# Kernel tuning notes

Hardware: AMD Instinct MI355X
Metric: run time of the kernel (lower is better)

## Reference

```python
import jax, jax.numpy as jnp
import numpy as np

B, T, D = 8, 4096, 1280   # batch, frames, feature dim
Q, K = 4, 256             # num_quantizers, codebook_size


def setup_inputs() -> dict:
    key = jax.random.key(0)
    k1, k2, k3 = jax.random.split(key, 3)
    z = jax.random.normal(k1, (B, T, D), jnp.float32)
    mask = jax.random.randint(k2, (B, T), 0, 2).astype(bool)
    codebooks = jax.random.normal(k3, (Q, K, D), jnp.float32)
    return {"z": z, "mask": mask, "codebooks": codebooks}


def _stage(residual, codebook):
    # squared L2 distance: ||r||^2 - 2 r.c + ||c||^2; ||r||^2 constant over codes -> drop for argmin
    dots = jnp.einsum('btd,kd->btk', residual, codebook)            # [B,T,K]
    d2 = jnp.sum(codebook * codebook, axis=-1) - 2.0 * dots          # [B,T,K]
    idx = jnp.argmin(d2, axis=-1)                                    # [B,T]
    q = codebook[idx]                                                # gather -> [B,T,D]
    return idx, q


def reference(z, mask, codebooks):
    residual = z
    quantized_out = jnp.zeros_like(z)
    commit = jnp.zeros((), z.dtype)
    mf = mask.astype(z.dtype)                                        # [B,T]
    denom = jnp.maximum(jnp.sum(mf), 1.0)
    indices = []
    for qi in range(codebooks.shape[0]):
        idx, q = _stage(residual, codebooks[qi])
        q_sg = jax.lax.stop_gradient(q)
        # straight-through estimator, as in vector-quantize-pytorch
        q_st = residual + jax.lax.stop_gradient(q - residual)
        quantized_out = quantized_out + q_st
        # masked commitment loss (MSE to detached codes, averaged over valid frames)
        se = jnp.mean((residual - q_sg) ** 2, axis=-1)               # [B,T]
        commit = commit + jnp.sum(se * mf) / denom
        # residual for next stage uses detached quantized (EMA codebooks)
        residual = residual - q_sg
        indices.append(idx)
    indices = jnp.stack(indices, axis=-1)                            # [B,T,Q]
    return quantized_out, indices, commit
```

## Files before the change

### kernel.cpp

```cpp
#include <hip/hip_runtime.h>
#include <hip/hip_bf16.h>
#include <float.h>

#define ROWS 32768
#define D4 320
#define QQ 4
#define KK 256
#define QUANT_N (ROWS*1280)
#define IDX_OFF QUANT_N
#define COMMIT_OFF (IDX_OFF + ROWS*QQ)
#define WIN 0.05f
#define TAU 3.0e-4

#define WS_CBT      0
#define WS_CN32     5242880
#define WS_CN64     5246976
#define WS_DENOM    5255168
#define WS_MODE     5255172
#define WS_COUNTS   5255176
#define WS_KFINAL   5255200
#define WS_FLAGGED  5386272
#define WS_SEROW    5517344
#define WS_CBH      6041632
#define WS_CBL      8663072

typedef __attribute__((ext_vector_type(8))) short bf16x8;
typedef __attribute__((ext_vector_type(4))) float f32x4;

__device__ __forceinline__ float xmul(float a, float b) {
    float r;
    asm("v_mul_f32 %0, %1, %2" : "=v"(r) : "v"(a), "v"(b));
    return r;
}
__device__ __forceinline__ float npadd(float a, float b) { return a + b; }

__device__ __forceinline__ float combine8(const float* r) {
    float t1 = npadd(r[0], r[1]), t2 = npadd(r[2], r[3]);
    float t3 = npadd(r[4], r[5]), t4 = npadd(r[6], r[7]);
    return npadd(npadd(t1, t2), npadd(t3, t4));
}
__device__ __forceinline__ float tree16(const float* L) {
    float p160[8];
#pragma unroll
    for (int h = 0; h < 8; ++h) p160[h] = npadd(L[2*h], L[2*h+1]);
    float p320[4];
#pragma unroll
    for (int h = 0; h < 4; ++h) p320[h] = npadd(p160[2*h], p160[2*h+1]);
    return npadd(npadd(p320[0], p320[1]), npadd(p320[2], p320[3]));
}

__device__ __forceinline__ unsigned short bfrne(float x) {
    unsigned u = __float_as_uint(x);
    unsigned r = (u + 0x7FFFu + ((u >> 16) & 1u)) >> 16;
    return (unsigned short)r;
}
__device__ __forceinline__ void split2(float x, unsigned short &h, unsigned short &l) {
    unsigned u = __float_as_uint(x);
    unsigned r = (u + 0x7FFFu + ((u >> 16) & 1u)) >> 16;
    h = (unsigned short)r;
    float hf = __uint_as_float(r << 16);
    float d = x - hf;
    unsigned u2 = __float_as_uint(d);
    unsigned r2 = (u2 + 0x7FFFu + ((u2 >> 16) & 1u)) >> 16;
    l = (unsigned short)r2;
}

__global__ void k_mask(const unsigned int* mw, float* denom_out, int* mode_out,
                       int* counts) {
    __shared__ unsigned int s_or;
    __shared__ int warp_s[4];
    int t = threadIdx.x;
    if (t == 0) s_or = 0;
    __syncthreads();
    unsigned int orv = 0;
    for (int i = t; i < 8192; i += 256) orv |= mw[i];
    atomicOr(&s_or, orv);
    __syncthreads();
    const unsigned int o = s_or;
    int mode;
    if ((o & ~0x01010101u) == 0u && o > 1u) mode = 1;
    else if (o <= 1u) mode = 0;
    else mode = 2;
    int s = 0;
    if (mode == 1) {
        for (int i = t; i < 8192; i += 256) s += __popc(mw[i] & 0x01010101u);
    } else if (mode == 0) {
        for (int i = t; i < ROWS; i += 256) s += (int)mw[i];
    } else {
        for (int i = t; i < ROWS; i += 256) s += (mw[i] == 0x3F800000u) ? 1 : 0;
    }
    for (int off = 32; off; off >>= 1) s += __shfl_down(s, off);
    if ((t & 63) == 0) warp_s[t >> 6] = s;
    __syncthreads();
    if (t == 0) {
        int tot = warp_s[0] + warp_s[1] + warp_s[2] + warp_s[3];
        *denom_out = fmaxf((float)tot, 1.0f);
        *mode_out = mode;
        counts[0] = 0; counts[1] = 0; counts[2] = 0; counts[3] = 0;
    }
}

__device__ __forceinline__ float mask_val(const unsigned int* mw, int mode, int grow) {
    if (mode == 1) return (float)((const unsigned char*)mw)[grow];
    if (mode == 0) return (float)((const int*)mw)[grow];
    return ((const float*)mw)[grow];
}

__global__ void k_cb(const float4* __restrict__ cb4, float4* __restrict__ cbT4,
                     float* __restrict__ cn32, double* __restrict__ cn64) {
    int blk = blockIdx.x;
    int q = blk >> 8, kk = blk & 255;
    int t = threadIdx.x;
    for (int i = t; i < 320; i += 64)
        cbT4[(size_t)(q * D4 + i) * KK + kk] = cb4[(size_t)(q * KK + kk) * D4 + i];

    const float* a = (const float*)(cb4 + (size_t)(q * KK + kk) * D4);

    __shared__ float leafs[16];
    __shared__ double dred[64];
    if (t < 16) {
        const float* al = a + t * 80;
        float rr[8];
#pragma unroll
        for (int j = 0; j < 8; ++j) rr[j] = xmul(al[j], al[j]);
        for (int g = 1; g < 10; ++g)
#pragma unroll
            for (int j = 0; j < 8; ++j) {
                float x = al[g * 8 + j];
                rr[j] = npadd(rr[j], xmul(x, x));
            }
        leafs[t] = combine8(rr);
    }
    double ds = 0.0;
    for (int i = t; i < 1280; i += 64) {
        double x = (double)a[i];
        ds = fma(x, x, ds);
    }
    dred[t] = ds;
    __syncthreads();
    if (t == 0) {
        cn32[q * KK + kk] = tree16(leafs);
        double s = 0.0;
        for (int i = 0; i < 64; ++i) s += dred[i];
        cn64[q * KK + kk] = s;
    }
}

__global__ void k_cbsplit(const float4* __restrict__ cb4,
                          unsigned short* __restrict__ cbh,
                          unsigned short* __restrict__ cbl) {
    int idx = blockIdx.x * 256 + threadIdx.x;
    float4 v = cb4[idx];
    ushort4 h, l;
    split2(v.x, h.x, l.x);
    split2(v.y, h.y, l.y);
    split2(v.z, h.z, l.z);
    split2(v.w, h.w, l.w);
    *(ushort4*)(cbh + (size_t)idx * 4) = h;
    *(ushort4*)(cbl + (size_t)idx * 4) = l;
}

__global__ __launch_bounds__(256, 1) void k_score(
    const float* __restrict__ resin,
    const unsigned short* __restrict__ cbh,
    const unsigned short* __restrict__ cbl,
    const float* __restrict__ cn32,
    int* __restrict__ kfinal, int* __restrict__ flagged, int* __restrict__ counts,
    int q) {
    const int tid = threadIdx.x;
    const int lane = tid & 63;
    const int wv = tid >> 6;
    const int l15 = lane & 15, l4 = lane >> 4;
    const int row0 = blockIdx.x * 128;

    __shared__ unsigned short Ah[128 * 40];
    __shared__ unsigned short Al[128 * 40];
    __shared__ unsigned short Bh[256 * 40];
    __shared__ unsigned short Bl[256 * 40];
    __shared__ float cn_s[256];

    cn_s[tid] = cn32[q * 256 + tid];

    const float4* resin4 = (const float4*)resin;
    const unsigned short* cbhq = cbh + (size_t)q * 256 * 1280;
    const unsigned short* cblq = cbl + (size_t)q * 256 * 1280;

    f32x4 acc0[16], acc1[16];
#pragma unroll
    for (int ct = 0; ct < 16; ++ct) {
        acc0[ct] = (f32x4){0.f, 0.f, 0.f, 0.f};
        acc1[ct] = (f32x4){0.f, 0.f, 0.f, 0.f};
    }

    float4 avr[4];
    uint4  bhr[4], blr[4];

#define LOADSTEP(KS)                                                          \
    {                                                                         \
        _Pragma("unroll")                                                     \
        for (int i = 0; i < 4; ++i) {                                         \
            int idx = i * 256 + tid;                                          \
            int row = idx >> 3, c4 = idx & 7;                                 \
            avr[i] = resin4[(size_t)(row0 + row) * D4 + (KS) * 8 + c4];       \
        }                                                                     \
        _Pragma("unroll")                                                     \
        for (int i = 0; i < 4; ++i) {                                         \
            int idx = i * 256 + tid;                                          \
            int code = idx >> 2, ch = idx & 3;                                \
            size_t e = (size_t)code * 1280 + (KS) * 32 + ch * 8;              \
            bhr[i] = *(const uint4*)(cbhq + e);                               \
            blr[i] = *(const uint4*)(cblq + e);                               \
        }                                                                     \
    }

#define WRITESTEP()                                                           \
    {                                                                         \
        _Pragma("unroll")                                                     \
        for (int i = 0; i < 4; ++i) {                                         \
            int idx = i * 256 + tid;                                          \
            int row = idx >> 3, c4 = idx & 7;                                 \
            ushort4 h, l;                                                     \
            split2(avr[i].x, h.x, l.x);                                       \
            split2(avr[i].y, h.y, l.y);                                       \
            split2(avr[i].z, h.z, l.z);                                       \
            split2(avr[i].w, h.w, l.w);                                       \
            *(ushort4*)(&Ah[row * 40 + c4 * 4]) = h;                          \
            *(ushort4*)(&Al[row * 40 + c4 * 4]) = l;                          \
        }                                                                     \
        _Pragma("unroll")                                                     \
        for (int i = 0; i < 4; ++i) {                                         \
            int idx = i * 256 + tid;                                          \
            int code = idx >> 2, ch = idx & 3;                                \
            *(uint4*)(&Bh[code * 40 + ch * 8]) = bhr[i];                      \
            *(uint4*)(&Bl[code * 40 + ch * 8]) = blr[i];                      \
        }                                                                     \
    }

    LOADSTEP(0);
    WRITESTEP();

    for (int ks = 0; ks < 40; ++ks) {
        __syncthreads();
        if (ks + 1 < 40) LOADSTEP(ks + 1);
        bf16x8 ah0 = *(const bf16x8*)(&Ah[(wv * 32 + l15) * 40 + l4 * 8]);
        bf16x8 ah1 = *(const bf16x8*)(&Ah[(wv * 32 + 16 + l15) * 40 + l4 * 8]);
        bf16x8 al0 = *(const bf16x8*)(&Al[(wv * 32 + l15) * 40 + l4 * 8]);
        bf16x8 al1 = *(const bf16x8*)(&Al[(wv * 32 + 16 + l15) * 40 + l4 * 8]);
#pragma unroll
        for (int ct = 0; ct < 16; ++ct) {
            bf16x8 bh = *(const bf16x8*)(&Bh[(ct * 16 + l15) * 40 + l4 * 8]);
            bf16x8 bl = *(const bf16x8*)(&Bl[(ct * 16 + l15) * 40 + l4 * 8]);
            acc0[ct] = __builtin_amdgcn_mfma_f32_16x16x32_bf16(ah0, bh, acc0[ct], 0, 0, 0);
            acc0[ct] = __builtin_amdgcn_mfma_f32_16x16x32_bf16(ah0, bl, acc0[ct], 0, 0, 0);
            acc0[ct] = __builtin_amdgcn_mfma_f32_16x16x32_bf16(al0, bh, acc0[ct], 0, 0, 0);
            acc1[ct] = __builtin_amdgcn_mfma_f32_16x16x32_bf16(ah1, bh, acc1[ct], 0, 0, 0);
            acc1[ct] = __builtin_amdgcn_mfma_f32_16x16x32_bf16(ah1, bl, acc1[ct], 0, 0, 0);
            acc1[ct] = __builtin_amdgcn_mfma_f32_16x16x32_bf16(al1, bh, acc1[ct], 0, 0, 0);
        }
        __syncthreads();
        if (ks + 1 < 40) WRITESTEP();
    }

#pragma unroll
    for (int rt = 0; rt < 2; ++rt) {
#pragma unroll
        for (int r = 0; r < 4; ++r) {
            float v1 = FLT_MAX, v2 = FLT_MAX;
            int k1 = 0;
#pragma unroll
            for (int ct = 0; ct < 16; ++ct) {
                f32x4 a4 = rt ? acc1[ct] : acc0[ct];
                float d2 = fmaf(-2.0f, a4[r], cn_s[ct * 16 + l15]);
                if (d2 < v1) { v2 = v1; v1 = d2; k1 = ct * 16 + l15; }
                else v2 = fminf(v2, d2);
            }
#pragma unroll
            for (int off = 1; off < 16; off <<= 1) {
                float pv1 = __shfl_xor(v1, off, 16);
                int   pk1 = __shfl_xor(k1, off, 16);
                float pv2 = __shfl_xor(v2, off, 16);
                if (pv1 < v1 || (pv1 == v1 && pk1 < k1)) {
                    v2 = fminf(v1, pv2); v1 = pv1; k1 = pk1;
                } else {
                    v2 = fminf(v2, pv1);
                }
            }
            if (l15 == 0) {
                int grow = row0 + wv * 32 + rt * 16 + l4 * 4 + r;
                kfinal[grow] = k1;
                if (v2 - v1 < WIN) {
                    int pos = atomicAdd(&counts[q], 1);
                    flagged[pos] = grow;
                }
            }
        }
    }
#undef LOADSTEP
#undef WRITESTEP
}

__global__ __launch_bounds__(256) void k_fixup(
    const float4* __restrict__ resin4,
    const float4* __restrict__ cbT4,
    const float* __restrict__ cn32,
    const double* __restrict__ cn64,
    const int* __restrict__ flagged, const int* __restrict__ counts,
    int* __restrict__ kfinal, int q) {
    __shared__ float4 srow[4][320];
    __shared__ double sd2[4][256];
    __shared__ float  sc2[4][256];
    __shared__ int    rows_s[4];
    const int n = counts[q];
    const int k = threadIdx.x;
    const double cnd = cn64[q * 256 + k];
    const float  cnf = cn32[q * 256 + k];
    for (int base = blockIdx.x * 4; base < n; base += gridDim.x * 4) {
        const int cnt = min(4, n - base);
        __syncthreads();
        if (k < cnt) rows_s[k] = flagged[base + k];
        __syncthreads();
        for (int idx = k; idx < cnt * 320; idx += 256) {
            int r = idx / 320, c4 = idx % 320;
            srow[r][c4] = resin4[(size_t)rows_s[r] * D4 + c4];
        }
        __syncthreads();
        for (int r = 0; r < cnt; ++r) {
            double dot64 = 0.0;
            float dotc = 0.0f;
            for (int c4 = 0; c4 < 320; ++c4) {
                float4 a = srow[r][c4];
                float4 b = cbT4[(size_t)(q * D4 + c4) * KK + k];
                dot64 = fma((double)a.x, (double)b.x, dot64);
                dot64 = fma((double)a.y, (double)b.y, dot64);
                dot64 = fma((double)a.z, (double)b.z, dot64);
                dot64 = fma((double)a.w, (double)b.w, dot64);
                dotc = fmaf(a.x, b.x, dotc);
                dotc = fmaf(a.y, b.y, dotc);
                dotc = fmaf(a.z, b.z, dotc);
                dotc = fmaf(a.w, b.w, dotc);
            }
            sd2[r][k] = cnd - 2.0 * dot64;
            sc2[r][k] = fmaf(-2.0f, dotc, cnf);
        }
        __syncthreads();
        if (k < cnt) {
            double va = sd2[k][0], vb = 1.0e300;
            int a = 0, b = -1;
            for (int kk2 = 1; kk2 < 256; ++kk2) {
                double x = sd2[k][kk2];
                if (x < va) { vb = va; b = a; va = x; a = kk2; }
                else if (x < vb) { vb = x; b = kk2; }
            }
            float vc = sc2[k][0];
            int c = 0;
            for (int kk2 = 1; kk2 < 256; ++kk2) {
                float x = sc2[k][kk2];
                if (x < vc) { vc = x; c = kk2; }
            }
            int pick = a;
            if ((vb - va) < (double)TAU && c == a && b >= 0) pick = b;
            kfinal[rows_s[k]] = pick;
        }
        __syncthreads();
    }
}

__global__ __launch_bounds__(256) void k_update(
    const float4* __restrict__ resin4, float4* __restrict__ resout4,
    const float4* __restrict__ cb4, const int* __restrict__ kfinal,
    const unsigned int* __restrict__ maskw, const int* __restrict__ mode_p,
    float* __restrict__ out_idx, float* __restrict__ serow, int q) {
    const int tid = threadIdx.x;
    const int row0 = blockIdx.x * 8;
    __shared__ float s_nr[8][1296];
    __shared__ float s_leaf[8][16];
    __shared__ int   s_k[8];

    if (tid < 8) {
        int kk = kfinal[row0 + tid];
        s_k[tid] = kk;
        out_idx[(size_t)(row0 + tid) * QQ + q] = (float)kk;
    }
    __syncthreads();

#pragma unroll
    for (int it = 0; it < 10; ++it) {
        int f = it * 256 + tid;
        int r = f / 320, c4 = f % 320;
        float4 a = resin4[(size_t)(row0 + r) * D4 + c4];
        float4 cv = cb4[((size_t)(q * KK + s_k[r])) * D4 + c4];
        float4 nr = make_float4(a.x - cv.x, a.y - cv.y, a.z - cv.z, a.w - cv.w);
        resout4[(size_t)(row0 + r) * D4 + c4] = nr;
        float vals[4] = {nr.x, nr.y, nr.z, nr.w};
#pragma unroll
        for (int j = 0; j < 4; ++j) {
            int d = c4 * 4 + j;
            int leaf = d / 80, i = d - leaf * 80;
            s_nr[r][leaf * 81 + i] = vals[j];
        }
    }
    __syncthreads();

    if (tid < 128) {
        int r = tid >> 4, leaf = tid & 15;
        const float* a = &s_nr[r][leaf * 81];
        float rr[8];
#pragma unroll
        for (int j = 0; j < 8; ++j) rr[j] = xmul(a[j], a[j]);
        for (int g = 1; g < 10; ++g)
#pragma unroll
            for (int j = 0; j < 8; ++j) {
                float x = a[g * 8 + j];
                rr[j] = npadd(rr[j], xmul(x, x));
            }
        s_leaf[r][leaf] = combine8(rr);
    }
    __syncthreads();

    if (tid < 8) {
        int grow = row0 + tid;
        float tot = tree16(s_leaf[tid]);
        float se = tot / 1280.0f;
        float mf = mask_val(maskw, *mode_p, grow);
        serow[q * ROWS + grow] = xmul(se, mf);
    }
}

__global__ void k_final(const float4* __restrict__ z4, float4* __restrict__ out4) {
    size_t i = (size_t)blockIdx.x * blockDim.x + threadIdx.x;
    size_t stride = (size_t)gridDim.x * blockDim.x;
    for (; i < (size_t)QUANT_N / 4; i += stride) {
        float4 z = z4[i], r = out4[i];
        out4[i] = make_float4(z.x - r.x, z.y - r.y, z.z - r.z, z.w - r.w);
    }
}

__global__ void k_commit(const float* __restrict__ serow,
                         const float* __restrict__ denom_p,
                         float* __restrict__ commit_out) {
    __shared__ float red[256];
    int t = threadIdx.x;
    float dn = *denom_p;
    float c0 = 0.0f;
    for (int q = 0; q < 4; ++q) {
        const float* a = serow + q * ROWS + t * 128;
        float r[8];
#pragma unroll
        for (int j = 0; j < 8; ++j) r[j] = a[j];
        for (int i = 8; i < 128; i += 8)
#pragma unroll
            for (int j = 0; j < 8; ++j) r[j] = npadd(r[j], a[i + j]);
        red[t] = combine8(r);
        __syncthreads();
        for (int width = 128; width >= 1; width >>= 1) {
            float v = 0.0f;
            if (t < width) v = npadd(red[2 * t], red[2 * t + 1]);
            __syncthreads();
            if (t < width) red[t] = v;
            __syncthreads();
        }
        if (t == 0) c0 = npadd(c0, red[0] / dn);
        __syncthreads();
    }
    if (t == 0) *commit_out = c0;
}

extern "C" void kernel_launch(void* const* d_in, const int* in_sizes, int n_in,
                              void* d_out, int out_size, void* d_ws, size_t ws_size,
                              hipStream_t stream) {
    const float* z = (const float*)d_in[0];
    const unsigned int* mask = (const unsigned int*)d_in[1];
    const float* cb = (const float*)d_in[2];
    float* out = (float*)d_out;

    char* ws = (char*)d_ws;
    float4* cbT4 = (float4*)(ws + WS_CBT);
    float* cn32 = (float*)(ws + WS_CN32);
    double* cn64 = (double*)(ws + WS_CN64);
    float* denom = (float*)(ws + WS_DENOM);
    int* mmode = (int*)(ws + WS_MODE);
    int* counts = (int*)(ws + WS_COUNTS);
    int* kfinal = (int*)(ws + WS_KFINAL);
    int* flagged = (int*)(ws + WS_FLAGGED);
    float* serow = (float*)(ws + WS_SEROW);
    unsigned short* cbh = (unsigned short*)(ws + WS_CBH);
    unsigned short* cbl = (unsigned short*)(ws + WS_CBL);

    float* oidx = out + IDX_OFF;
    float* commit = out + COMMIT_OFF;

    k_mask<<<1, 256, 0, stream>>>(mask, denom, mmode, counts);
    k_cb<<<QQ * KK, 64, 0, stream>>>((const float4*)cb, cbT4, cn32, cn64);
    k_cbsplit<<<1280, 256, 0, stream>>>((const float4*)cb, cbh, cbl);
    for (int q = 0; q < QQ; ++q) {
        const float* rin = (q == 0) ? z : out;
        k_score<<<ROWS / 128, 256, 0, stream>>>(rin, cbh, cbl, cn32, kfinal,
                                                flagged, counts, q);
        k_fixup<<<512, 256, 0, stream>>>((const float4*)rin, cbT4, cn32, cn64,
                                         flagged, counts, kfinal, q);
        k_update<<<ROWS / 8, 256, 0, stream>>>((const float4*)rin, (float4*)out,
                                               (const float4*)cb, kfinal, mask,
                                               mmode, oidx, serow, q);
    }
    k_final<<<2048, 256, 0, stream>>>((const float4*)z, (float4*)out);
    k_commit<<<1, 256, 0, stream>>>(serow, denom, commit);
}
```

Baseline: 1.495 ms.

## Drop codebook low-bf16 term, pre-swizzle codebook, widen fixup window, fuse final subtraction

The scoring GEMM now uses a two-term split (residual hi/lo times codebook hi) instead of three, so the codebook low-part buffer goes away. The codebook is pre-swizzled into MFMA fragment order, and tiles shrink to 64 rows with two blocks per CU. The near-tie window for exact fp64 fixup is widened from 0.05 to 1.25 so that more rows are rechecked, and the fixup kernel now processes four rows per codebook load. The last update stage writes z minus the residual directly, which removes the separate final pass. The trade is fewer MFMAs and less memory traffic against many more flagged rows going through the slow fixup path.

```diff
diff --git a/kernel.cpp b/kernel.cpp
--- a/kernel.cpp
+++ b/kernel.cpp
@@ -9,7 +9,7 @@
 #define QUANT_N (ROWS*1280)
 #define IDX_OFF QUANT_N
 #define COMMIT_OFF (IDX_OFF + ROWS*QQ)
-#define WIN 0.05f
+#define WIN 1.25f
 #define TAU 3.0e-4
 
 #define WS_CBT      0
@@ -22,7 +22,6 @@
 #define WS_FLAGGED  5386272
 #define WS_SEROW    5517344
 #define WS_CBH      6041632
-#define WS_CBL      8663072
 
 typedef __attribute__((ext_vector_type(8))) short bf16x8;
 typedef __attribute__((ext_vector_type(4))) float f32x4;
@@ -49,11 +48,6 @@
     return npadd(npadd(p320[0], p320[1]), npadd(p320[2], p320[3]));
 }
 
-__device__ __forceinline__ unsigned short bfrne(float x) {
-    unsigned u = __float_as_uint(x);
-    unsigned r = (u + 0x7FFFu + ((u >> 16) & 1u)) >> 16;
-    return (unsigned short)r;
-}
 __device__ __forceinline__ void split2(float x, unsigned short &h, unsigned short &l) {
     unsigned u = __float_as_uint(x);
     unsigned r = (u + 0x7FFFu + ((u >> 16) & 1u)) >> 16;
@@ -147,23 +141,28 @@
 }
 
 __global__ void k_cbsplit(const float4* __restrict__ cb4,
-                          unsigned short* __restrict__ cbh,
-                          unsigned short* __restrict__ cbl) {
+                          unsigned short* __restrict__ cbh) {
     int idx = blockIdx.x * 256 + threadIdx.x;
+    int q = idx / 81920;
+    int rem = idx - q * 81920;
+    int code = rem / 320, c4 = rem - code * 320;
     float4 v = cb4[idx];
     ushort4 h, l;
     split2(v.x, h.x, l.x);
     split2(v.y, h.y, l.y);
     split2(v.z, h.z, l.z);
     split2(v.w, h.w, l.w);
-    *(ushort4*)(cbh + (size_t)idx * 4) = h;
-    *(ushort4*)(cbl + (size_t)idx * 4) = l;
-}
-
-__global__ __launch_bounds__(256, 1) void k_score(
+    int ks = c4 >> 3;
+    int kgrp = (c4 >> 1) & 3;
+    int elem0 = (c4 & 1) * 4;
+    size_t dst = (size_t)q * 327680 + ks * 8192 + (code >> 4) * 512
+               + (kgrp * 16 + (code & 15)) * 8 + elem0;
+    *(ushort4*)(cbh + dst) = h;
+}
+
+__global__ __launch_bounds__(256, 2) void k_score(
     const float* __restrict__ resin,
     const unsigned short* __restrict__ cbh,
-    const unsigned short* __restrict__ cbl,
     const float* __restrict__ cn32,
     int* __restrict__ kfinal, int* __restrict__ flagged, int* __restrict__ counts,
     int q) {
@@ -171,52 +170,44 @@
     const int lane = tid & 63;
     const int wv = tid >> 6;
     const int l15 = lane & 15, l4 = lane >> 4;
-    const int row0 = blockIdx.x * 128;
-
-    __shared__ unsigned short Ah[128 * 40];
-    __shared__ unsigned short Al[128 * 40];
-    __shared__ unsigned short Bh[256 * 40];
-    __shared__ unsigned short Bl[256 * 40];
+    const int row0 = blockIdx.x * 64;
+
+    __shared__ unsigned short Ah[4 * 64 * 8];
+    __shared__ unsigned short Al[4 * 64 * 8];
+    __shared__ unsigned short Bh[16 * 64 * 8];
     __shared__ float cn_s[256];
 
     cn_s[tid] = cn32[q * 256 + tid];
 
     const float4* resin4 = (const float4*)resin;
-    const unsigned short* cbhq = cbh + (size_t)q * 256 * 1280;
-    const unsigned short* cblq = cbl + (size_t)q * 256 * 1280;
-
-    f32x4 acc0[16], acc1[16];
-#pragma unroll
-    for (int ct = 0; ct < 16; ++ct) {
-        acc0[ct] = (f32x4){0.f, 0.f, 0.f, 0.f};
-        acc1[ct] = (f32x4){0.f, 0.f, 0.f, 0.f};
-    }
-
-    float4 avr[4];
-    uint4  bhr[4], blr[4];
+    const unsigned short* cbq = cbh + (size_t)q * 327680;
+
+    f32x4 acc[16];
+#pragma unroll
+    for (int ct = 0; ct < 16; ++ct) acc[ct] = (f32x4){0.f, 0.f, 0.f, 0.f};
+
+    float4 avr[2];
+    uint4  bvr[4];
 
 #define LOADSTEP(KS)                                                          \
     {                                                                         \
         _Pragma("unroll")                                                     \
-        for (int i = 0; i < 4; ++i) {                                         \
+        for (int i = 0; i < 2; ++i) {                                         \
             int idx = i * 256 + tid;                                          \
             int row = idx >> 3, c4 = idx & 7;                                 \
             avr[i] = resin4[(size_t)(row0 + row) * D4 + (KS) * 8 + c4];       \
         }                                                                     \
         _Pragma("unroll")                                                     \
         for (int i = 0; i < 4; ++i) {                                         \
-            int idx = i * 256 + tid;                                          \
-            int code = idx >> 2, ch = idx & 3;                                \
-            size_t e = (size_t)code * 1280 + (KS) * 32 + ch * 8;              \
-            bhr[i] = *(const uint4*)(cbhq + e);                               \
-            blr[i] = *(const uint4*)(cblq + e);                               \
+            bvr[i] = *(const uint4*)(cbq + (size_t)(KS) * 8192                \
+                                     + (i * 256 + tid) * 8);                  \
         }                                                                     \
     }
 
-#define WRITESTEP()                                                           \
+#define WRITESTEP()                                                          \
     {                                                                         \
         _Pragma("unroll")                                                     \
-        for (int i = 0; i < 4; ++i) {                                         \
+        for (int i = 0; i < 2; ++i) {                                         \
             int idx = i * 256 + tid;                                          \
             int row = idx >> 3, c4 = idx & 7;                                 \
             ushort4 h, l;                                                     \
@@ -224,16 +215,14 @@
             split2(avr[i].y, h.y, l.y);                                       \
             split2(avr[i].z, h.z, l.z);                                       \
             split2(avr[i].w, h.w, l.w);                                       \
-            *(ushort4*)(&Ah[row * 40 + c4 * 4]) = h;                          \
-            *(ushort4*)(&Al[row * 40 + c4 * 4]) = l;                          \
+            int dst = ((row >> 4) * 64 + ((c4 >> 1) & 3) * 16 + (row & 15)) * 8 \
+                      + (c4 & 1) * 4;                                         \
+            *(ushort4*)(&Ah[dst]) = h;                                        \
+            *(ushort4*)(&Al[dst]) = l;                                        \
         }                                                                     \
         _Pragma("unroll")                                                     \
-        for (int i = 0; i < 4; ++i) {                                         \
-            int idx = i * 256 + tid;                                          \
-            int code = idx >> 2, ch = idx & 3;                                \
-            *(uint4*)(&Bh[code * 40 + ch * 8]) = bhr[i];                      \
-            *(uint4*)(&Bl[code * 40 + ch * 8]) = blr[i];                      \
-        }                                                                     \
+        for (int i = 0; i < 4; ++i)                                           \
+            *(uint4*)(&Bh[(i * 256 + tid) * 8]) = bvr[i];                     \
     }
 
     LOADSTEP(0);
@@ -242,56 +231,45 @@
     for (int ks = 0; ks < 40; ++ks) {
         __syncthreads();
         if (ks + 1 < 40) LOADSTEP(ks + 1);
-        bf16x8 ah0 = *(const bf16x8*)(&Ah[(wv * 32 + l15) * 40 + l4 * 8]);
-        bf16x8 ah1 = *(const bf16x8*)(&Ah[(wv * 32 + 16 + l15) * 40 + l4 * 8]);
-        bf16x8 al0 = *(const bf16x8*)(&Al[(wv * 32 + l15) * 40 + l4 * 8]);
-        bf16x8 al1 = *(const bf16x8*)(&Al[(wv * 32 + 16 + l15) * 40 + l4 * 8]);
+        bf16x8 ah = *(const bf16x8*)(&Ah[(wv * 64 + lane) * 8]);
+        bf16x8 al = *(const bf16x8*)(&Al[(wv * 64 + lane) * 8]);
 #pragma unroll
         for (int ct = 0; ct < 16; ++ct) {
-            bf16x8 bh = *(const bf16x8*)(&Bh[(ct * 16 + l15) * 40 + l4 * 8]);
-            bf16x8 bl = *(const bf16x8*)(&Bl[(ct * 16 + l15) * 40 + l4 * 8]);
-            acc0[ct] = __builtin_amdgcn_mfma_f32_16x16x32_bf16(ah0, bh, acc0[ct], 0, 0, 0);
-            acc0[ct] = __builtin_amdgcn_mfma_f32_16x16x32_bf16(ah0, bl, acc0[ct], 0, 0, 0);
-            acc0[ct] = __builtin_amdgcn_mfma_f32_16x16x32_bf16(al0, bh, acc0[ct], 0, 0, 0);
-            acc1[ct] = __builtin_amdgcn_mfma_f32_16x16x32_bf16(ah1, bh, acc1[ct], 0, 0, 0);
-            acc1[ct] = __builtin_amdgcn_mfma_f32_16x16x32_bf16(ah1, bl, acc1[ct], 0, 0, 0);
-            acc1[ct] = __builtin_amdgcn_mfma_f32_16x16x32_bf16(al1, bh, acc1[ct], 0, 0, 0);
+            bf16x8 bh = *(const bf16x8*)(&Bh[(ct * 64 + lane) * 8]);
+            acc[ct] = __builtin_amdgcn_mfma_f32_16x16x32_bf16(ah, bh, acc[ct], 0, 0, 0);
+            acc[ct] = __builtin_amdgcn_mfma_f32_16x16x32_bf16(al, bh, acc[ct], 0, 0, 0);
         }
         __syncthreads();
         if (ks + 1 < 40) WRITESTEP();
     }
 
 #pragma unroll
-    for (int rt = 0; rt < 2; ++rt) {
-#pragma unroll
-        for (int r = 0; r < 4; ++r) {
-            float v1 = FLT_MAX, v2 = FLT_MAX;
-            int k1 = 0;
-#pragma unroll
-            for (int ct = 0; ct < 16; ++ct) {
-                f32x4 a4 = rt ? acc1[ct] : acc0[ct];
-                float d2 = fmaf(-2.0f, a4[r], cn_s[ct * 16 + l15]);
-                if (d2 < v1) { v2 = v1; v1 = d2; k1 = ct * 16 + l15; }
-                else v2 = fminf(v2, d2);
-            }
-#pragma unroll
-            for (int off = 1; off < 16; off <<= 1) {
-                float pv1 = __shfl_xor(v1, off, 16);
-                int   pk1 = __shfl_xor(k1, off, 16);
-                float pv2 = __shfl_xor(v2, off, 16);
-                if (pv1 < v1 || (pv1 == v1 && pk1 < k1)) {
-                    v2 = fminf(v1, pv2); v1 = pv1; k1 = pk1;
-                } else {
-                    v2 = fminf(v2, pv1);
-                }
-            }
-            if (l15 == 0) {
-                int grow = row0 + wv * 32 + rt * 16 + l4 * 4 + r;
-                kfinal[grow] = k1;
-                if (v2 - v1 < WIN) {
-                    int pos = atomicAdd(&counts[q], 1);
-                    flagged[pos] = grow;
-                }
+    for (int r = 0; r < 4; ++r) {
+        float v1 = FLT_MAX, v2 = FLT_MAX;
+        int k1 = 0;
+#pragma unroll
+        for (int ct = 0; ct < 16; ++ct) {
+            float d2 = fmaf(-2.0f, acc[ct][r], cn_s[ct * 16 + l15]);
+            if (d2 < v1) { v2 = v1; v1 = d2; k1 = ct * 16 + l15; }
+            else v2 = fminf(v2, d2);
+        }
+#pragma unroll
+        for (int off = 1; off < 16; off <<= 1) {
+            float pv1 = __shfl_xor(v1, off, 16);
+            int   pk1 = __shfl_xor(k1, off, 16);
+            float pv2 = __shfl_xor(v2, off, 16);
+            if (pv1 < v1 || (pv1 == v1 && pk1 < k1)) {
+                v2 = fminf(v1, pv2); v1 = pv1; k1 = pk1;
+            } else {
+                v2 = fminf(v2, pv1);
+            }
+        }
+        if (l15 == 0) {
+            int grow = row0 + wv * 16 + l4 * 4 + r;
+            kfinal[grow] = k1;
+            if (v2 - v1 < WIN) {
+                int pos = atomicAdd(&counts[q], 1);
+                flagged[pos] = grow;
             }
         }
     }
@@ -317,30 +295,36 @@
     for (int base = blockIdx.x * 4; base < n; base += gridDim.x * 4) {
         const int cnt = min(4, n - base);
         __syncthreads();
-        if (k < cnt) rows_s[k] = flagged[base + k];
-        __syncthreads();
-        for (int idx = k; idx < cnt * 320; idx += 256) {
-            int r = idx / 320, c4 = idx % 320;
+        if (k < 4) rows_s[k] = flagged[min(base + k, n - 1)];
+        __syncthreads();
+        for (int idx = k; idx < 4 * 320; idx += 256) {
+            int r = idx >> 8 == 0 ? 0 : idx / 320;
+            r = idx / 320;
+            int c4 = idx - r * 320;
             srow[r][c4] = resin4[(size_t)rows_s[r] * D4 + c4];
         }
         __syncthreads();
-        for (int r = 0; r < cnt; ++r) {
-            double dot64 = 0.0;
-            float dotc = 0.0f;
-            for (int c4 = 0; c4 < 320; ++c4) {
+        double d64[4] = {0.0, 0.0, 0.0, 0.0};
+        float  dc[4] = {0.f, 0.f, 0.f, 0.f};
+        for (int c4 = 0; c4 < 320; ++c4) {
+            float4 b = cbT4[(size_t)(q * D4 + c4) * KK + k];
+#pragma unroll
+            for (int r = 0; r < 4; ++r) {
                 float4 a = srow[r][c4];
-                float4 b = cbT4[(size_t)(q * D4 + c4) * KK + k];
-                dot64 = fma((double)a.x, (double)b.x, dot64);
-                dot64 = fma((double)a.y, (double)b.y, dot64);
-                dot64 = fma((double)a.z, (double)b.z, dot64);
-                dot64 = fma((double)a.w, (double)b.w, dot64);
-                dotc = fmaf(a.x, b.x, dotc);
-                dotc = fmaf(a.y, b.y, dotc);
-                dotc = fmaf(a.z, b.z, dotc);
-                dotc = fmaf(a.w, b.w, dotc);
-            }
-            sd2[r][k] = cnd - 2.0 * dot64;
-            sc2[r][k] = fmaf(-2.0f, dotc, cnf);
+                d64[r] = fma((double)a.x, (double)b.x, d64[r]);
+                d64[r] = fma((double)a.y, (double)b.y, d64[r]);
+                d64[r] = fma((double)a.z, (double)b.z, d64[r]);
+                d64[r] = fma((double)a.w, (double)b.w, d64[r]);
+                dc[r] = fmaf(a.x, b.x, dc[r]);
+                dc[r] = fmaf(a.y, b.y, dc[r]);
+                dc[r] = fmaf(a.z, b.z, dc[r]);
+                dc[r] = fmaf(a.w, b.w, dc[r]);
+            }
+        }
+#pragma unroll
+        for (int r = 0; r < 4; ++r) {
+            sd2[r][k] = cnd - 2.0 * d64[r];
+            sc2[r][k] = fmaf(-2.0f, dc[r], cnf);
         }
         __syncthreads();
         if (k < cnt) {
@@ -367,6 +351,7 @@
 
 __global__ __launch_bounds__(256) void k_update(
     const float4* __restrict__ resin4, float4* __restrict__ resout4,
+    const float4* __restrict__ z4,
     const float4* __restrict__ cb4, const int* __restrict__ kfinal,
     const unsigned int* __restrict__ maskw, const int* __restrict__ mode_p,
     float* __restrict__ out_idx, float* __restrict__ serow, int q) {
@@ -383,14 +368,21 @@
     }
     __syncthreads();
 
+    const bool last = (q == QQ - 1);
 #pragma unroll
     for (int it = 0; it < 10; ++it) {
         int f = it * 256 + tid;
         int r = f / 320, c4 = f % 320;
-        float4 a = resin4[(size_t)(row0 + r) * D4 + c4];
+        size_t gi = (size_t)(row0 + r) * D4 + c4;
+        float4 a = resin4[gi];
         float4 cv = cb4[((size_t)(q * KK + s_k[r])) * D4 + c4];
         float4 nr = make_float4(a.x - cv.x, a.y - cv.y, a.z - cv.z, a.w - cv.w);
-        resout4[(size_t)(row0 + r) * D4 + c4] = nr;
+        if (last) {
+            float4 z = z4[gi];
+            resout4[gi] = make_float4(z.x - nr.x, z.y - nr.y, z.z - nr.z, z.w - nr.w);
+        } else {
+            resout4[gi] = nr;
+        }
         float vals[4] = {nr.x, nr.y, nr.z, nr.w};
 #pragma unroll
         for (int j = 0; j < 4; ++j) {
@@ -423,15 +415,6 @@
         float se = tot / 1280.0f;
         float mf = mask_val(maskw, *mode_p, grow);
         serow[q * ROWS + grow] = xmul(se, mf);
-    }
-}
-
-__global__ void k_final(const float4* __restrict__ z4, float4* __restrict__ out4) {
-    size_t i = (size_t)blockIdx.x * blockDim.x + threadIdx.x;
-    size_t stride = (size_t)gridDim.x * blockDim.x;
-    for (; i < (size_t)QUANT_N / 4; i += stride) {
-        float4 z = z4[i], r = out4[i];
-        out4[i] = make_float4(z.x - r.x, z.y - r.y, z.z - r.z, z.w - r.w);
     }
 }
 
@@ -484,24 +467,23 @@
     int* flagged = (int*)(ws + WS_FLAGGED);
     float* serow = (float*)(ws + WS_SEROW);
     unsigned short* cbh = (unsigned short*)(ws + WS_CBH);
-    unsigned short* cbl = (unsigned short*)(ws + WS_CBL);
 
     float* oidx = out + IDX_OFF;
     float* commit = out + COMMIT_OFF;
 
     k_mask<<<1, 256, 0, stream>>>(mask, denom, mmode, counts);
     k_cb<<<QQ * KK, 64, 0, stream>>>((const float4*)cb, cbT4, cn32, cn64);
-    k_cbsplit<<<1280, 256, 0, stream>>>((const float4*)cb, cbh, cbl);
+    k_cbsplit<<<1280, 256, 0, stream>>>((const float4*)cb, cbh);
     for (int q = 0; q < QQ; ++q) {
         const float* rin = (q == 0) ? z : out;
-        k_score<<<ROWS / 128, 256, 0, stream>>>(rin, cbh, cbl, cn32, kfinal,
-                                                flagged, counts, q);
+        k_score<<<ROWS / 64, 256, 0, stream>>>(rin, cbh, cn32, kfinal,
+                                               flagged, counts, q);
         k_fixup<<<512, 256, 0, stream>>>((const float4*)rin, cbT4, cn32, cn64,
                                          flagged, counts, kfinal, q);
         k_update<<<ROWS / 8, 256, 0, stream>>>((const float4*)rin, (float4*)out,
+                                               (const float4*)z,
                                                (const float4*)cb, kfinal, mask,
                                                mmode, oidx, serow, q);
     }
-    k_final<<<2048, 256, 0, stream>>>((const float4*)z, (float4*)out);
     k_commit<<<1, 256, 0, stream>>>(serow, denom, commit);
 }
```

Result: slower. 1.768 ms (+18.2%).
